# Kernel optimization log

Hardware: AMD Instinct MI355X
Metric: run time of the kernel (lower is better)

The kernel has to match this reference:

```python
import jax, jax.numpy as jnp
import numpy as np

NUM_WIRES = 4
NUM_LAYERS = 2


def _apply_ry(state, w, theta):
    # state: (N, 2,2,2,2); theta: scalar or (N,)
    st = jnp.moveaxis(state, 1 + w, -1)
    c = jnp.cos(theta / 2)
    s = jnp.sin(theta / 2)
    # broadcast (N,) -> (N,1,1,1) against st[...,k] of shape (N,2,2,2)
    c = c.reshape(c.shape + (1,) * (st.ndim - 1 - c.ndim))
    s = s.reshape(s.shape + (1,) * (st.ndim - 1 - s.ndim))
    a0, a1 = st[..., 0], st[..., 1]
    st = jnp.stack([c * a0 - s * a1, s * a0 + c * a1], axis=-1)
    return jnp.moveaxis(st, -1, 1 + w)


def _apply_rz(state, w, theta):
    st = jnp.moveaxis(state, 1 + w, -1)
    p = jnp.exp(-0.5j * theta)  # phase on |0>; conj on |1>
    st = jnp.stack([st[..., 0] * p, st[..., 1] * jnp.conj(p)], axis=-1)
    return jnp.moveaxis(st, -1, 1 + w)


def _apply_cnot(state, cw, tw):
    st = jnp.moveaxis(state, (1 + cw, 1 + tw), (-2, -1))
    st = jnp.stack([st[..., 0, :], st[..., 1, ::-1]], axis=-2)
    return jnp.moveaxis(st, (-2, -1), (1 + cw, 1 + tw))


def _circuit(angles, params):
    # angles: (N, 4) RY input angles; params: (L, 4, 3)
    N = angles.shape[0]
    state = jnp.zeros((N, 2, 2, 2, 2), jnp.complex64).at[:, 0, 0, 0, 0].set(1.0)
    for i in range(NUM_WIRES):
        state = _apply_ry(state, i, angles[:, i])
    for l in range(NUM_LAYERS):
        for i in range(NUM_WIRES):
            state = _apply_ry(state, i, params[l, i, 0])
        for i in range(NUM_WIRES - 1):
            state = _apply_cnot(state, i, i + 1)
        for i in range(NUM_WIRES):
            state = _apply_ry(state, i, params[l, i, 1])
        for i in range(NUM_WIRES - 1):
            state = _apply_cnot(state, i + 1, i)
        for i in range(NUM_WIRES):
            state = _apply_rz(state, i, params[l, i, 2])
    probs = state.real ** 2 + state.imag ** 2  # (N,2,2,2,2)
    zs = []
    for i in range(NUM_WIRES):
        axes = tuple(a for a in range(1, 1 + NUM_WIRES) if a != 1 + i)
        marg = probs.sum(axis=axes)  # (N,2)
        zs.append(marg[:, 0] - marg[:, 1])
    return jnp.stack(zs, axis=1)  # (N,4)


def setup_inputs() -> dict:
    key = jax.random.key(0)
    kx, kp = jax.random.split(key)
    x = jax.random.normal(kx, (512, 28, 28), dtype=jnp.float32)
    params = jax.random.normal(kp, (NUM_LAYERS, NUM_WIRES, 3), dtype=jnp.float32)
    return {"x": x, "params": params}


def reference(x, params):
    B = x.shape[0]
    # extract non-overlapping 2x2 patches, row-major over (r, c), patch order
    # [x[r,c], x[r,c+1], x[r+1,c], x[r+1,c+1]] matching .view(batch, -1)
    patches = x.reshape(B, 14, 2, 14, 2).transpose(0, 1, 3, 2, 4).reshape(B, 196, 4)
    # per-patch-location scalar normalization over all batch*4 elements (ddof=1 std)
    n = B * 4
    m = patches.mean(axis=(0, 2), keepdims=True)
    sd = jnp.sqrt(((patches - m) ** 2).sum(axis=(0, 2), keepdims=True) / (n - 1))
    angles = (patches - m) / (sd + 1e-8) * jnp.pi
    z = _circuit(angles.reshape(B * 196, 4), params)  # (B*196, 4)
    return z.reshape(B, 196 * 4).astype(jnp.float32)
```

## Files before the change

kernel.cpp:

```cpp
#include <hip/hip_runtime.h>
#include <math.h>

#define BATCH   512
#define NPATCH  196

template <int MASK>
__device__ __forceinline__ void ry_gate(float* sr, float* si, float c, float s) {
    #pragma unroll
    for (int i = 0; i < 16; ++i) {
        if ((i & MASK) == 0) {
            const int j = i | MASK;
            float a0 = sr[i], a1 = sr[j];
            sr[i] = c * a0 - s * a1;
            sr[j] = s * a0 + c * a1;
            float b0 = si[i], b1 = si[j];
            si[i] = c * b0 - s * b1;
            si[j] = s * b0 + c * b1;
        }
    }
}

template <int CMASK, int TMASK>
__device__ __forceinline__ void cnot_gate(float* sr, float* si) {
    #pragma unroll
    for (int i = 0; i < 16; ++i) {
        if ((i & CMASK) && !(i & TMASK)) {
            const int j = i | TMASK;
            float t;
            t = sr[i]; sr[i] = sr[j]; sr[j] = t;
            t = si[i]; si[i] = si[j]; si[j] = t;
        }
    }
}

template <int MASK>
__device__ __forceinline__ void rz_gate(float* sr, float* si, float pc, float ps) {
    #pragma unroll
    for (int i = 0; i < 16; ++i) {
        float r = sr[i], im = si[i];
        if (i & MASK) { sr[i] = r * pc - im * ps; si[i] = im * pc + r * ps; }
        else          { sr[i] = r * pc + im * ps; si[i] = im * pc - r * ps; }
    }
}

__device__ __forceinline__ float4 run_circuit(float h0, float h1, float h2, float h3,
                                              const float* GC, const float* GS) {
    float c0, s0, c1, s1, c2, s2, c3, s3;
    __sincosf(h0, &s0, &c0);
    __sincosf(h1, &s1, &c1);
    __sincosf(h2, &s2, &c2);
    __sincosf(h3, &s3, &c3);

    float sr[16], si[16];
    #pragma unroll
    for (int i = 0; i < 16; ++i) {
        sr[i] = ((i & 8) ? s0 : c0) * ((i & 4) ? s1 : c1) *
                ((i & 2) ? s2 : c2) * ((i & 1) ? s3 : c3);
        si[i] = 0.0f;
    }

    #pragma unroll
    for (int l = 0; l < 2; ++l) {
        const int o = l * 12;
        ry_gate<8>(sr, si, GC[o + 0], GS[o + 0]);
        ry_gate<4>(sr, si, GC[o + 3], GS[o + 3]);
        ry_gate<2>(sr, si, GC[o + 6], GS[o + 6]);
        ry_gate<1>(sr, si, GC[o + 9], GS[o + 9]);
        cnot_gate<8, 4>(sr, si);
        cnot_gate<4, 2>(sr, si);
        cnot_gate<2, 1>(sr, si);
        ry_gate<8>(sr, si, GC[o + 1],  GS[o + 1]);
        ry_gate<4>(sr, si, GC[o + 4],  GS[o + 4]);
        ry_gate<2>(sr, si, GC[o + 7],  GS[o + 7]);
        ry_gate<1>(sr, si, GC[o + 10], GS[o + 10]);
        cnot_gate<4, 8>(sr, si);
        cnot_gate<2, 4>(sr, si);
        cnot_gate<1, 2>(sr, si);
        rz_gate<8>(sr, si, GC[o + 2],  GS[o + 2]);
        rz_gate<4>(sr, si, GC[o + 5],  GS[o + 5]);
        rz_gate<2>(sr, si, GC[o + 8],  GS[o + 8]);
        rz_gate<1>(sr, si, GC[o + 11], GS[o + 11]);
    }

    float z0 = 0.f, z1 = 0.f, z2 = 0.f, z3 = 0.f;
    #pragma unroll
    for (int i = 0; i < 16; ++i) {
        float pr = sr[i] * sr[i] + si[i] * si[i];
        z0 += (i & 8) ? -pr : pr;
        z1 += (i & 4) ? -pr : pr;
        z2 += (i & 2) ? -pr : pr;
        z3 += (i & 1) ? -pr : pr;
    }
    return make_float4(z0, z1, z2, z3);
}

__global__ __launch_bounds__(256) void fused_kernel(const float* __restrict__ x,
                                                    const float* __restrict__ params,
                                                    float* __restrict__ out) {
    __shared__ float s_gc[24], s_gs[24];
    __shared__ float s_sum[4], s_sq[4];
    __shared__ float s_m, s_invh;

    const int p = blockIdx.x;
    const int r = p / 14, c = p - r * 14;
    const int t = threadIdx.x;

    if (t < 24) {
        float gs, gc;
        __sincosf(0.5f * params[t], &gs, &gc);
        s_gc[t] = gc;
        s_gs[t] = gs;
    }

    const float* base0 = x + t * 784 + (2 * r) * 28 + 2 * c;
    float2 a01 = *(const float2*)base0;
    float2 a23 = *(const float2*)(base0 + 28);
    const float* base1 = base0 + 256 * 784;
    float2 b01 = *(const float2*)base1;
    float2 b23 = *(const float2*)(base1 + 28);

    float sum = a01.x + a01.y + a23.x + a23.y + b01.x + b01.y + b23.x + b23.y;
    float sq  = a01.x * a01.x + a01.y * a01.y + a23.x * a23.x + a23.y * a23.y
              + b01.x * b01.x + b01.y * b01.y + b23.x * b23.x + b23.y * b23.y;

    #pragma unroll
    for (int off = 32; off; off >>= 1) {
        sum += __shfl_down(sum, off, 64);
        sq  += __shfl_down(sq,  off, 64);
    }
    const int wave = t >> 6, lane = t & 63;
    if (lane == 0) { s_sum[wave] = sum; s_sq[wave] = sq; }
    __syncthreads();
    if (t == 0) {
        float S = s_sum[0] + s_sum[1] + s_sum[2] + s_sum[3];
        float Q = s_sq[0]  + s_sq[1]  + s_sq[2]  + s_sq[3];
        const float n = (float)(BATCH * 4);
        float m   = S / n;
        float var = (Q - S * S / n) / (n - 1.0f);
        float sd  = sqrtf(fmaxf(var, 0.f));
        s_m    = m;
        s_invh = 0.5f * 3.14159265358979323846f / (sd + 1e-8f);
    }
    __syncthreads();

    const float m    = s_m;
    const float invh = s_invh;

    float GC[24], GS[24];
    #pragma unroll
    for (int i = 0; i < 24; ++i) { GC[i] = s_gc[i]; GS[i] = s_gs[i]; }

    float4 z = run_circuit((a01.x - m) * invh, (a01.y - m) * invh,
                           (a23.x - m) * invh, (a23.y - m) * invh, GC, GS);
    *(float4*)(out + t * (NPATCH * 4) + p * 4) = z;

    z = run_circuit((b01.x - m) * invh, (b01.y - m) * invh,
                    (b23.x - m) * invh, (b23.y - m) * invh, GC, GS);
    *(float4*)(out + (t + 256) * (NPATCH * 4) + p * 4) = z;
}

extern "C" void kernel_launch(void* const* d_in, const int* in_sizes, int n_in,
                              void* d_out, int out_size, void* d_ws, size_t ws_size,
                              hipStream_t stream) {
    const float* x      = (const float*)d_in[0];
    const float* params = (const float*)d_in[1];
    float*       out    = (float*)d_out;

    fused_kernel<<<NPATCH, 256, 0, stream>>>(x, params, out);
}
```

Measured before the change: 63.84 us.

## Exploit real-valued first layer, merge RZ phases, drop final RZ layer

```diff
diff --git a/kernel.cpp b/kernel.cpp
--- a/kernel.cpp
+++ b/kernel.cpp
@@ -4,24 +4,49 @@
 #define BATCH   512
 #define NPATCH  196
 
+
 template <int MASK>
-__device__ __forceinline__ void ry_gate(float* sr, float* si, float c, float s) {
-    #pragma unroll
-    for (int i = 0; i < 16; ++i) {
-        if ((i & MASK) == 0) {
+__device__ __forceinline__ void ry_real(float* s, float c, float sn) {
+    #pragma unroll
+    for (int i = 0; i < 16; ++i) {
+        if (!(i & MASK)) {
+            const int j = i | MASK;
+            float a0 = s[i], a1 = s[j];
+            s[i] = c * a0 - sn * a1;
+            s[j] = sn * a0 + c * a1;
+        }
+    }
+}
+
+template <int MASK>
+__device__ __forceinline__ void ry_cplx(float* sr, float* si, float c, float sn) {
+    #pragma unroll
+    for (int i = 0; i < 16; ++i) {
+        if (!(i & MASK)) {
             const int j = i | MASK;
             float a0 = sr[i], a1 = sr[j];
-            sr[i] = c * a0 - s * a1;
-            sr[j] = s * a0 + c * a1;
+            sr[i] = c * a0 - sn * a1;
+            sr[j] = sn * a0 + c * a1;
             float b0 = si[i], b1 = si[j];
-            si[i] = c * b0 - s * b1;
-            si[j] = s * b0 + c * b1;
+            si[i] = c * b0 - sn * b1;
+            si[j] = sn * b0 + c * b1;
         }
     }
 }
 
 template <int CMASK, int TMASK>
-__device__ __forceinline__ void cnot_gate(float* sr, float* si) {
+__device__ __forceinline__ void cnot_real(float* s) {
+    #pragma unroll
+    for (int i = 0; i < 16; ++i) {
+        if ((i & CMASK) && !(i & TMASK)) {
+            const int j = i | TMASK;
+            float t = s[i]; s[i] = s[j]; s[j] = t;
+        }
+    }
+}
+
+template <int CMASK, int TMASK>
+__device__ __forceinline__ void cnot_cplx(float* sr, float* si) {
     #pragma unroll
     for (int i = 0; i < 16; ++i) {
         if ((i & CMASK) && !(i & TMASK)) {
@@ -33,96 +58,44 @@
     }
 }
 
-template <int MASK>
-__device__ __forceinline__ void rz_gate(float* sr, float* si, float pc, float ps) {
-    #pragma unroll
-    for (int i = 0; i < 16; ++i) {
-        float r = sr[i], im = si[i];
-        if (i & MASK) { sr[i] = r * pc - im * ps; si[i] = im * pc + r * ps; }
-        else          { sr[i] = r * pc + im * ps; si[i] = im * pc - r * ps; }
-    }
-}
-
-__device__ __forceinline__ float4 run_circuit(float h0, float h1, float h2, float h3,
-                                              const float* GC, const float* GS) {
-    float c0, s0, c1, s1, c2, s2, c3, s3;
-    __sincosf(h0, &s0, &c0);
-    __sincosf(h1, &s1, &c1);
-    __sincosf(h2, &s2, &c2);
-    __sincosf(h3, &s3, &c3);
-
-    float sr[16], si[16];
-    #pragma unroll
-    for (int i = 0; i < 16; ++i) {
-        sr[i] = ((i & 8) ? s0 : c0) * ((i & 4) ? s1 : c1) *
-                ((i & 2) ? s2 : c2) * ((i & 1) ? s3 : c3);
-        si[i] = 0.0f;
-    }
-
-    #pragma unroll
-    for (int l = 0; l < 2; ++l) {
-        const int o = l * 12;
-        ry_gate<8>(sr, si, GC[o + 0], GS[o + 0]);
-        ry_gate<4>(sr, si, GC[o + 3], GS[o + 3]);
-        ry_gate<2>(sr, si, GC[o + 6], GS[o + 6]);
-        ry_gate<1>(sr, si, GC[o + 9], GS[o + 9]);
-        cnot_gate<8, 4>(sr, si);
-        cnot_gate<4, 2>(sr, si);
-        cnot_gate<2, 1>(sr, si);
-        ry_gate<8>(sr, si, GC[o + 1],  GS[o + 1]);
-        ry_gate<4>(sr, si, GC[o + 4],  GS[o + 4]);
-        ry_gate<2>(sr, si, GC[o + 7],  GS[o + 7]);
-        ry_gate<1>(sr, si, GC[o + 10], GS[o + 10]);
-        cnot_gate<4, 8>(sr, si);
-        cnot_gate<2, 4>(sr, si);
-        cnot_gate<1, 2>(sr, si);
-        rz_gate<8>(sr, si, GC[o + 2],  GS[o + 2]);
-        rz_gate<4>(sr, si, GC[o + 5],  GS[o + 5]);
-        rz_gate<2>(sr, si, GC[o + 8],  GS[o + 8]);
-        rz_gate<1>(sr, si, GC[o + 11], GS[o + 11]);
-    }
-
-    float z0 = 0.f, z1 = 0.f, z2 = 0.f, z3 = 0.f;
-    #pragma unroll
-    for (int i = 0; i < 16; ++i) {
-        float pr = sr[i] * sr[i] + si[i] * si[i];
-        z0 += (i & 8) ? -pr : pr;
-        z1 += (i & 4) ? -pr : pr;
-        z2 += (i & 2) ? -pr : pr;
-        z3 += (i & 1) ? -pr : pr;
-    }
-    return make_float4(z0, z1, z2, z3);
-}
-
-__global__ __launch_bounds__(256) void fused_kernel(const float* __restrict__ x,
+__global__ __launch_bounds__(512) void fused_kernel(const float* __restrict__ x,
                                                     const float* __restrict__ params,
                                                     float* __restrict__ out) {
-    __shared__ float s_gc[24], s_gs[24];
-    __shared__ float s_sum[4], s_sq[4];
+    __shared__ float s_ryc[16], s_rys[16];
+    __shared__ float s_pc[16], s_ps[16];
+    __shared__ float s_sum[8], s_sq[8];
     __shared__ float s_m, s_invh;
 
     const int p = blockIdx.x;
     const int r = p / 14, c = p - r * 14;
     const int t = threadIdx.x;
 
-    if (t < 24) {
-        float gs, gc;
-        __sincosf(0.5f * params[t], &gs, &gc);
-        s_gc[t] = gc;
-        s_gs[t] = gs;
-    }
-
-    const float* base0 = x + t * 784 + (2 * r) * 28 + 2 * c;
-    float2 a01 = *(const float2*)base0;
-    float2 a23 = *(const float2*)(base0 + 28);
-    const float* base1 = base0 + 256 * 784;
-    float2 b01 = *(const float2*)base1;
-    float2 b23 = *(const float2*)(base1 + 28);
-
-    float sum = a01.x + a01.y + a23.x + a23.y + b01.x + b01.y + b23.x + b23.y;
-    float sq  = a01.x * a01.x + a01.y * a01.y + a23.x * a23.x + a23.y * a23.y
-              + b01.x * b01.x + b01.y * b01.y + b23.x * b23.x + b23.y * b23.y;
-
+    if (t < 16) {
+        const int l = t >> 3, set = (t >> 2) & 1, w = t & 3;
+        float sn, cs;
+        __sincosf(0.5f * params[l * 12 + w * 3 + set], &sn, &cs);
+        s_ryc[t] = cs;
+        s_rys[t] = sn;
+    } else if (t < 32) {
+        const int i = t - 16;
+        const float h0 = 0.5f * params[0 * 3 + 2];
+        const float h1 = 0.5f * params[1 * 3 + 2];
+        const float h2 = 0.5f * params[2 * 3 + 2];
+        const float h3 = 0.5f * params[3 * 3 + 2];
+        const float alpha = ((i & 8) ? h0 : -h0) + ((i & 4) ? h1 : -h1)
+                          + ((i & 2) ? h2 : -h2) + ((i & 1) ? h3 : -h3);
+        float sn, cs;
+        __sincosf(alpha, &sn, &cs);
+        s_pc[i] = cs;
+        s_ps[i] = sn;
+    }
+
+    const float* base = x + t * 784 + (2 * r) * 28 + 2 * c;
+    const float2 a01 = *(const float2*)base;
+    const float2 a23 = *(const float2*)(base + 28);
+
+    float sum = a01.x + a01.y + a23.x + a23.y;
+    float sq  = a01.x * a01.x + a01.y * a01.y + a23.x * a23.x + a23.y * a23.y;
     #pragma unroll
     for (int off = 32; off; off >>= 1) {
         sum += __shfl_down(sum, off, 64);
@@ -132,8 +105,9 @@
     if (lane == 0) { s_sum[wave] = sum; s_sq[wave] = sq; }
     __syncthreads();
     if (t == 0) {
-        float S = s_sum[0] + s_sum[1] + s_sum[2] + s_sum[3];
-        float Q = s_sq[0]  + s_sq[1]  + s_sq[2]  + s_sq[3];
+        float S = 0.f, Q = 0.f;
+        #pragma unroll
+        for (int w = 0; w < 8; ++w) { S += s_sum[w]; Q += s_sq[w]; }
         const float n = (float)(BATCH * 4);
         float m   = S / n;
         float var = (Q - S * S / n) / (n - 1.0f);
@@ -146,25 +120,95 @@
     const float m    = s_m;
     const float invh = s_invh;
 
-    float GC[24], GS[24];
-    #pragma unroll
-    for (int i = 0; i < 24; ++i) { GC[i] = s_gc[i]; GS[i] = s_gs[i]; }
-
-    float4 z = run_circuit((a01.x - m) * invh, (a01.y - m) * invh,
-                           (a23.x - m) * invh, (a23.y - m) * invh, GC, GS);
-    *(float4*)(out + t * (NPATCH * 4) + p * 4) = z;
-
-    z = run_circuit((b01.x - m) * invh, (b01.y - m) * invh,
-                    (b23.x - m) * invh, (b23.y - m) * invh, GC, GS);
-    *(float4*)(out + (t + 256) * (NPATCH * 4) + p * 4) = z;
+    float c0, s0, c1, s1, c2, s2, c3, s3;
+    __sincosf((a01.x - m) * invh, &s0, &c0);
+    __sincosf((a01.y - m) * invh, &s1, &c1);
+    __sincosf((a23.x - m) * invh, &s2, &c2);
+    __sincosf((a23.y - m) * invh, &s3, &c3);
+
+    float sr[16];
+    {
+        const float cc01 = c0 * c1, cs01 = c0 * s1, sc01 = s0 * c1, ss01 = s0 * s1;
+        const float cc23 = c2 * c3, cs23 = c2 * s3, sc23 = s2 * c3, ss23 = s2 * s3;
+        #pragma unroll
+        for (int i = 0; i < 16; ++i) {
+            const float hi = (i & 8) ? ((i & 4) ? ss01 : sc01) : ((i & 4) ? cs01 : cc01);
+            const float lo = (i & 2) ? ((i & 1) ? ss23 : sc23) : ((i & 1) ? cs23 : cc23);
+            sr[i] = hi * lo;
+        }
+    }
+
+    ry_real<8>(sr, s_ryc[0], s_rys[0]);
+    ry_real<4>(sr, s_ryc[1], s_rys[1]);
+    ry_real<2>(sr, s_ryc[2], s_rys[2]);
+    ry_real<1>(sr, s_ryc[3], s_rys[3]);
+    cnot_real<8, 4>(sr);
+    cnot_real<4, 2>(sr);
+    cnot_real<2, 1>(sr);
+    ry_real<8>(sr, s_ryc[4], s_rys[4]);
+    ry_real<4>(sr, s_ryc[5], s_rys[5]);
+    ry_real<2>(sr, s_ryc[6], s_rys[6]);
+    ry_real<1>(sr, s_ryc[7], s_rys[7]);
+    cnot_real<4, 8>(sr);
+    cnot_real<2, 4>(sr);
+    cnot_real<1, 2>(sr);
+
+    float si[16];
+    #pragma unroll
+    for (int i = 0; i < 16; ++i) {
+        si[i] = sr[i] * s_ps[i];
+        sr[i] = sr[i] * s_pc[i];
+    }
+
+    ry_cplx<8>(sr, si, s_ryc[8],  s_rys[8]);
+    ry_cplx<4>(sr, si, s_ryc[9],  s_rys[9]);
+    ry_cplx<2>(sr, si, s_ryc[10], s_rys[10]);
+    ry_cplx<1>(sr, si, s_ryc[11], s_rys[11]);
+    cnot_cplx<8, 4>(sr, si);
+    cnot_cplx<4, 2>(sr, si);
+    cnot_cplx<2, 1>(sr, si);
+    ry_cplx<8>(sr, si, s_ryc[12], s_rys[12]);
+    ry_cplx<4>(sr, si, s_ryc[13], s_rys[13]);
+    ry_cplx<2>(sr, si, s_ryc[14], s_rys[14]);
+    ry_cplx<1>(sr, si, s_ryc[15], s_rys[15]);
+    cnot_cplx<4, 8>(sr, si);
+    cnot_cplx<2, 4>(sr, si);
+    cnot_cplx<1, 2>(sr, si);
+
+    float pr[16];
+    #pragma unroll
+    for (int i = 0; i < 16; ++i) pr[i] = sr[i] * sr[i] + si[i] * si[i];
+
+    float a[8], z3 = 0.f;
+    #pragma unroll
+    for (int k = 0; k < 8; ++k) {
+        a[k] = pr[2 * k] + pr[2 * k + 1];
+        z3  += pr[2 * k] - pr[2 * k + 1];
+    }
+    float b[4], z2 = 0.f;
+    #pragma unroll
+    for (int k = 0; k < 4; ++k) {
+        b[k] = a[2 * k] + a[2 * k + 1];
+        z2  += a[2 * k] - a[2 * k + 1];
+    }
+    float g2[2], z1 = 0.f;
+    #pragma unroll
+    for (int k = 0; k < 2; ++k) {
+        g2[k] = b[2 * k] + b[2 * k + 1];
+        z1   += b[2 * k] - b[2 * k + 1];
+    }
+    const float z0 = g2[0] - g2[1];
+
+    *(float4*)(out + t * (NPATCH * 4) + p * 4) = make_float4(z0, z1, z2, z3);
 }
 
 extern "C" void kernel_launch(void* const* d_in, const int* in_sizes, int n_in,
                               void* d_out, int out_size, void* d_ws, size_t ws_size,
                               hipStream_t stream) {
+    (void)in_sizes; (void)n_in; (void)d_ws; (void)ws_size; (void)out_size;
     const float* x      = (const float*)d_in[0];
     const float* params = (const float*)d_in[1];
     float*       out    = (float*)d_out;
 
-    fused_kernel<<<NPATCH, 256, 0, stream>>>(x, params, out);
-}
+    fused_kernel<<<NPATCH, 512, 0, stream>>>(x, params, out);
+}
```

Measured after the change: 61.83 us. 1.03x faster.
